# Kernel optimization log

Measured on AMD Instinct MI355X. Metric: run time of the kernel, lower is better.

## Reference

```python
import jax, jax.numpy as jnp
import numpy as np

B, S, D, H = 2, 2048, 1024, 16
HD = D // H
EPS = 1e-5

def gelu_tanh(x):
    # GPT-2 tanh approximation of GELU
    c = np.sqrt(2.0 / np.pi).astype(np.float32)
    return 0.5 * x * (1.0 + jnp.tanh(c * (x + 0.044715 * x * x * x)))

def layernorm(x, gamma, beta):
    mu = jnp.mean(x, axis=-1, keepdims=True)
    var = jnp.mean(jnp.square(x - mu), axis=-1, keepdims=True)
    return (x - mu) * jax.lax.rsqrt(var + EPS) * gamma + beta

def setup_inputs() -> dict:
    key = jax.random.key(0)
    ks = jax.random.split(key, 16)
    std = 0.02
    def w(k, shape):
        return jax.random.normal(k, shape, dtype=jnp.float32) * std
    return {
        "x": jax.random.normal(ks[0], (B, S, D), dtype=jnp.float32),
        "Wq": w(ks[1], (D, D)), "bq": jnp.zeros((D,), jnp.float32),
        "Wk": w(ks[2], (D, D)), "bk": jnp.zeros((D,), jnp.float32),
        "Wv": w(ks[3], (D, D)), "bv": jnp.zeros((D,), jnp.float32),
        "Wp": w(ks[4], (D, D)), "bp": jnp.zeros((D,), jnp.float32),
        "g0": jnp.ones((D,), jnp.float32), "beta0": jnp.zeros((D,), jnp.float32),
        "W1": w(ks[5], (D, 4 * D)), "b1": jnp.zeros((4 * D,), jnp.float32),
        "W2": w(ks[6], (4 * D, D)), "b2": jnp.zeros((D,), jnp.float32),
        "g1": jnp.ones((D,), jnp.float32), "beta1": jnp.zeros((D,), jnp.float32),
    }

def reference(x, Wq, bq, Wk, bk, Wv, bv, Wp, bp, g0, beta0, W1, b1, W2, b2, g1, beta1):
    b, s, d = x.shape
    # --- causal self-attention (naive full score matrix, as in source) ---
    q = (x @ Wq + bq).reshape(b, s, H, HD).transpose(0, 2, 1, 3)  # [b,h,s,hd]
    k = (x @ Wk + bk).reshape(b, s, H, HD).transpose(0, 2, 1, 3)
    v = (x @ Wv + bv).reshape(b, s, H, HD).transpose(0, 2, 1, 3)
    scores = jnp.einsum('bhqd,bhkd->bhqk', q, k) * (1.0 / np.sqrt(HD))
    mask = jnp.tril(jnp.ones((s, s), dtype=x.dtype))  # lower-triangular causal mask
    scores = scores * mask - 1e10 * (1.0 - mask)
    attn = jax.nn.softmax(scores, axis=-1)
    y = jnp.einsum('bhqk,bhkd->bhqd', attn, v)
    y = y.transpose(0, 2, 1, 3).reshape(b, s, d)
    a = y @ Wp + bp
    # --- post-LN MLP block ---
    x = x + a
    h = layernorm(x, g0, beta0)
    h = gelu_tanh(h @ W1 + b1)
    h = h @ W2 + b2
    x = x + h
    return layernorm(x, g1, beta1)
```

## Files before the change

### kernel.cpp

```cpp
#include <hip/hip_runtime.h>
#include <stdint.h>

#define S_LEN 2048
#define DIM   1024
#define NH    16
#define HDIM  64
#define MTOK  4096
#define DFF   4096

#define QS 0.18033688011112042f

typedef short bf16x8 __attribute__((ext_vector_type(8)));
typedef float f32x4  __attribute__((ext_vector_type(4)));
typedef float f32x16 __attribute__((ext_vector_type(16)));
typedef unsigned int u32x4 __attribute__((ext_vector_type(4)));

__device__ __forceinline__ unsigned short f2bf(float f) {
  unsigned int u = __float_as_uint(f);
  u += 0x7fffu + ((u >> 16) & 1u);
  return (unsigned short)(u >> 16);
}

__device__ __forceinline__ unsigned cvtpk(float a, float b) {
  unsigned r;
  asm("v_cvt_pk_bf16_f32 %0, %1, %2" : "=v"(r) : "v"(a), "v"(b));
  return r;
}

__device__ __forceinline__ float gelu_f(float x) {
  const float c = 0.7978845608028654f;
  float u = c * (x + 0.044715f * x * x * x);
  return 0.5f * x * (1.0f + tanhf(u));
}

__device__ __forceinline__ void gld_lds16(const void* g, void* lds) {
  using gu32p = __attribute__((address_space(1))) unsigned int*;
  using lu32p = __attribute__((address_space(3))) unsigned int*;
  __builtin_amdgcn_global_load_lds((gu32p)g, (lu32p)lds, 16, 0, 0);
}

__global__ __launch_bounds__(256) void cast_f32_bf16(const float* __restrict__ x,
                                                     unsigned short* __restrict__ xb) {
  const size_t i = (size_t)blockIdx.x * 256 + threadIdx.x;
  const float4 a = ((const float4*)x)[2 * i];
  const float4 b = ((const float4*)x)[2 * i + 1];
  ushort4 p0, p1;
  p0.x = f2bf(a.x); p0.y = f2bf(a.y); p0.z = f2bf(a.z); p0.w = f2bf(a.w);
  p1.x = f2bf(b.x); p1.y = f2bf(b.y); p1.z = f2bf(b.z); p1.w = f2bf(b.w);
  ((ushort4*)xb)[2 * i]     = p0;
  ((ushort4*)xb)[2 * i + 1] = p1;
}

__global__ __launch_bounds__(256) void tcast_k(const float* __restrict__ W,
                                               unsigned short* __restrict__ Wt,
                                               int K, int N, float scale) {
  __shared__ float tile[32][33];
  const int tx = threadIdx.x & 31, ty = threadIdx.x >> 5;
  const int n0 = blockIdx.x * 32, k0 = blockIdx.y * 32;
#pragma unroll
  for (int i = 0; i < 4; i++)
    tile[ty + 8 * i][tx] = W[(size_t)(k0 + ty + 8 * i) * N + n0 + tx];
  __syncthreads();
#pragma unroll
  for (int i = 0; i < 4; i++)
    Wt[(size_t)(n0 + ty + 8 * i) * K + k0 + tx] = f2bf(tile[tx][ty + 8 * i] * scale);
}

__global__ __launch_bounds__(256) void bcat_k(const float* __restrict__ bq,
                                              const float* __restrict__ bk,
                                              const float* __restrict__ bv,
                                              float* __restrict__ bqkv) {
  const int t = blockIdx.x * 256 + threadIdx.x;
  float v;
  if (t < 1024)      v = bq[t] * QS;
  else if (t < 2048) v = bk[t - 1024];
  else               v = bv[t - 2048];
  bqkv[t] = v;
}

__global__ __launch_bounds__(256) void vtrans_k(const unsigned short* __restrict__ qkv,
                                                unsigned short* __restrict__ vT) {
  __shared__ unsigned short tile[64][65];
  const int bh = blockIdx.y, b = bh >> 4, h = bh & 15;
  const int s0 = blockIdx.x * 64;
  const int t = threadIdx.x;
#pragma unroll
  for (int i = 0; i < 16; i++) {
    int idx = i * 256 + t, r = idx >> 6, c = idx & 63;
    tile[r][c] = qkv[(size_t)(b * S_LEN + s0 + r) * 3072 + 2048 + h * HDIM + c];
  }
  __syncthreads();
#pragma unroll
  for (int i = 0; i < 16; i++) {
    int idx = i * 256 + t, d = idx >> 6, s = idx & 63;
    vT[(size_t)(bh * HDIM + d) * S_LEN + s0 + s] = tile[s][d];
  }
}

template <int EPI>
__global__ __launch_bounds__(256, 2) void gemm2p(const unsigned short* __restrict__ A,
                                                 const unsigned short* __restrict__ Bt,
                                                 const float* __restrict__ bias,
                                                 const float* __restrict__ resid,
                                                 void* __restrict__ Cout,
                                                 int M, int N, int K) {
  __shared__ alignas(16) short As[2][128 * 64];
  __shared__ alignas(16) short Bs[2][128 * 64];
  const int t = threadIdx.x, w = t >> 6, lane = t & 63;

  const int gx = gridDim.x, nwg = gx * gridDim.y;
  const int bid = blockIdx.x + gx * blockIdx.y;
  const int swz = (bid & 7) * (nwg >> 3) + (bid >> 3);
  const int m0 = (swz / gx) * 128, n0 = (swz % gx) * 128;

  const int wr = (w >> 1) * 64, wc = (w & 1) * 64;
  const int lr = lane & 15, lg = lane >> 4;

  f32x4 acc[4][4] = {};

  const int sr = w * 32 + (lane >> 3);
  const int sc = (lane & 7) * 8;
  const unsigned short* Ag = A + (size_t)(m0 + sr) * K + sc;
  const unsigned short* Bg = Bt + (size_t)(n0 + sr) * K + sc;
  const int dbase = w * 4096 + lane * 16;

  const int NT = K >> 6;

#pragma unroll
  for (int i = 0; i < 4; i++) {
    gld_lds16(Ag + (size_t)(i * 8) * K, (char*)As[0] + dbase + i * 1024);
    gld_lds16(Bg + (size_t)(i * 8) * K, (char*)Bs[0] + dbase + i * 1024);
  }
  __syncthreads();

  int cur = 0;
  for (int kt = 0; kt < NT; ++kt) {
    if (kt + 1 < NT) {
      const int k1 = (kt + 1) << 6;
#pragma unroll
      for (int i = 0; i < 4; i++) {
        gld_lds16(Ag + (size_t)(i * 8) * K + k1, (char*)As[cur ^ 1] + dbase + i * 1024);
        gld_lds16(Bg + (size_t)(i * 8) * K + k1, (char*)Bs[cur ^ 1] + dbase + i * 1024);
      }
    }
    bf16x8 af[2][4], bfr[2][4];
#pragma unroll
    for (int ks = 0; ks < 2; ks++)
#pragma unroll
      for (int i = 0; i < 4; i++) {
        af[ks][i]  = *reinterpret_cast<const bf16x8*>(&As[cur][(wr + i * 16 + lr) * 64 + ks * 32 + lg * 8]);
        bfr[ks][i] = *reinterpret_cast<const bf16x8*>(&Bs[cur][(wc + i * 16 + lr) * 64 + ks * 32 + lg * 8]);
      }
    __builtin_amdgcn_s_setprio(1);
#pragma unroll
    for (int ks = 0; ks < 2; ks++)
#pragma unroll
      for (int mi = 0; mi < 4; mi++)
#pragma unroll
        for (int ni = 0; ni < 4; ni++)
          acc[mi][ni] = __builtin_amdgcn_mfma_f32_16x16x32_bf16(af[ks][mi], bfr[ks][ni],
                                                                acc[mi][ni], 0, 0, 0);
    __builtin_amdgcn_s_setprio(0);
    __syncthreads();
    cur ^= 1;
  }

  const int colb = n0 + wc + lr;
  const int rowb = m0 + wr + lg * 4;
#pragma unroll
  for (int ni = 0; ni < 4; ni++) {
    const int col = colb + ni * 16;
    const float bv = bias[col];
#pragma unroll
    for (int mi = 0; mi < 4; mi++) {
#pragma unroll
      for (int j = 0; j < 4; j++) {
        const int row = rowb + mi * 16 + j;
        const size_t idx = (size_t)row * N + col;
        float v = acc[mi][ni][j] + bv;
        if constexpr (EPI == 0) {
          ((unsigned short*)Cout)[idx] = f2bf(v);
        } else if constexpr (EPI == 1) {
          ((unsigned short*)Cout)[idx] = f2bf(gelu_f(v));
        } else {
          ((float*)Cout)[idx] = v + resid[idx];
        }
      }
    }
  }
}

__global__ __launch_bounds__(128) void attn32_k(const unsigned short* __restrict__ qkv,
                                                const unsigned short* __restrict__ vT,
                                                unsigned short* __restrict__ y) {
  __shared__ float smem[2][64][33];
  __shared__ float msh[2][64], lsh[2][64];

  const int t = threadIdx.x, w = t >> 6, lane = t & 63;
  const int ql = lane & 31, hi = lane >> 5;
  const int bh = blockIdx.x, bb = bh >> 4, hh = bh & 15;
  const int qt = 63 - blockIdx.y;
  const int half = w;
  const int q0 = qt * 32;

  const unsigned short* qp = qkv + (size_t)(bb * S_LEN + q0 + ql) * 3072 + hh * HDIM + hi * 8;
  const bf16x8 qf0 = *(const bf16x8*)(qp);
  const bf16x8 qf1 = *(const bf16x8*)(qp + 16);
  const bf16x8 qf2 = *(const bf16x8*)(qp + 32);
  const bf16x8 qf3 = *(const bf16x8*)(qp + 48);

  const unsigned short* kbp = qkv + (size_t)(bb * S_LEN) * 3072 + 1024 + hh * HDIM + hi * 8;
  const unsigned short* vbp = vT + (size_t)(bh * HDIM + ql) * (size_t)S_LEN + hi * 8;

  f32x16 acc0 = {}, acc1 = {};
  float m = -1e30f, l = 0.f;

  const int start = half * 32;

  const unsigned short* kp0 = kbp + (size_t)(start + ql) * 3072;
  bf16x8 kc0 = *(const bf16x8*)(kp0);
  bf16x8 kc1 = *(const bf16x8*)(kp0 + 16);
  bf16x8 kc2 = *(const bf16x8*)(kp0 + 32);
  bf16x8 kc3 = *(const bf16x8*)(kp0 + 48);

  for (int t0 = start; t0 <= q0; t0 += 64) {
    const unsigned short* vp = vbp + t0;
    const bf16x8 vf0 = *(const bf16x8*)(vp);
    const bf16x8 vf1 = *(const bf16x8*)(vp + 32 * S_LEN);
    const bf16x8 vf2 = *(const bf16x8*)(vp + 16);
    const bf16x8 vf3 = *(const bf16x8*)(vp + 32 * S_LEN + 16);

    __builtin_amdgcn_s_setprio(1);
    f32x16 st = {};
    st = __builtin_amdgcn_mfma_f32_32x32x16_bf16(kc0, qf0, st, 0, 0, 0);
    st = __builtin_amdgcn_mfma_f32_32x32x16_bf16(kc1, qf1, st, 0, 0, 0);
    st = __builtin_amdgcn_mfma_f32_32x32x16_bf16(kc2, qf2, st, 0, 0, 0);
    st = __builtin_amdgcn_mfma_f32_32x32x16_bf16(kc3, qf3, st, 0, 0, 0);
    __builtin_amdgcn_s_setprio(0);

    const int t1 = (t0 + 64 <= q0) ? (t0 + 64) : t0;
    const unsigned short* kpn = kbp + (size_t)(t1 + ql) * 3072;
    const bf16x8 kn0 = *(const bf16x8*)(kpn);
    const bf16x8 kn1 = *(const bf16x8*)(kpn + 16);
    const bf16x8 kn2 = *(const bf16x8*)(kpn + 32);
    const bf16x8 kn3 = *(const bf16x8*)(kpn + 48);

    if (t0 == q0) {
#pragma unroll
      for (int r = 0; r < 16; r++) {
        const int key = (r & 3) + 8 * (r >> 2) + 4 * hi;
        if (key > ql) st[r] = -1e30f;
      }
    }
    float pm = st[0];
#pragma unroll
    for (int r = 1; r < 16; r++) pm = fmaxf(pm, st[r]);
    pm = fmaxf(pm, __shfl_xor(pm, 32));
    if (!__all(pm - m <= 8.f)) {
      const float mn = fmaxf(m, pm);
      const float rs = exp2f(m - mn);
      l *= rs;
#pragma unroll
      for (int r = 0; r < 16; r++) { acc0[r] *= rs; acc1[r] *= rs; }
      m = mn;
    }
    float sum = 0.f;
#pragma unroll
    for (int r = 0; r < 16; r++) { st[r] = exp2f(st[r] - m); sum += st[r]; }
    sum += __shfl_xor(sum, 32);
    l += sum;

    {
      const unsigned c0 = cvtpk(st[0], st[1]), c1 = cvtpk(st[2], st[3]);
      const unsigned c2 = cvtpk(st[4], st[5]), c3 = cvtpk(st[6], st[7]);
      const unsigned x0 = __shfl_xor(c0, 32), x1 = __shfl_xor(c1, 32);
      const unsigned x2 = __shfl_xor(c2, 32), x3 = __shfl_xor(c3, 32);
      u32x4 fu;
      fu.x = hi ? x2 : c0; fu.y = hi ? x3 : c1;
      fu.z = hi ? c2 : x0; fu.w = hi ? c3 : x1;
      const bf16x8 pf = __builtin_bit_cast(bf16x8, fu);
      __builtin_amdgcn_s_setprio(1);
      acc0 = __builtin_amdgcn_mfma_f32_32x32x16_bf16(vf0, pf, acc0, 0, 0, 0);
      acc1 = __builtin_amdgcn_mfma_f32_32x32x16_bf16(vf1, pf, acc1, 0, 0, 0);
      __builtin_amdgcn_s_setprio(0);
    }
    {
      const unsigned c4 = cvtpk(st[8], st[9]),   c5 = cvtpk(st[10], st[11]);
      const unsigned c6 = cvtpk(st[12], st[13]), c7 = cvtpk(st[14], st[15]);
      const unsigned x4 = __shfl_xor(c4, 32), x5 = __shfl_xor(c5, 32);
      const unsigned x6 = __shfl_xor(c6, 32), x7 = __shfl_xor(c7, 32);
      u32x4 fu;
      fu.x = hi ? x6 : c4; fu.y = hi ? x7 : c5;
      fu.z = hi ? c6 : x4; fu.w = hi ? c7 : x5;
      const bf16x8 pf = __builtin_bit_cast(bf16x8, fu);
      __builtin_amdgcn_s_setprio(1);
      acc0 = __builtin_amdgcn_mfma_f32_32x32x16_bf16(vf2, pf, acc0, 0, 0, 0);
      acc1 = __builtin_amdgcn_mfma_f32_32x32x16_bf16(vf3, pf, acc1, 0, 0, 0);
      __builtin_amdgcn_s_setprio(0);
    }
    kc0 = kn0; kc1 = kn1; kc2 = kn2; kc3 = kn3;
  }

#pragma unroll
  for (int r = 0; r < 16; r++) {
    smem[w][lane][r]      = acc0[r];
    smem[w][lane][16 + r] = acc1[r];
  }
  msh[w][lane] = m; lsh[w][lane] = l;
  __syncthreads();
  if (half) return;

  const int pw = w ^ 1;
  const float mB = msh[pw][lane], lB = lsh[pw][lane];
  const float mm = fmaxf(m, mB);
  float sA = exp2f(m - mm), sB = exp2f(mB - mm);
  const float linv = 1.f / (l * sA + lB * sB);
  sA *= linv; sB *= linv;

  unsigned* tp = (unsigned*)&smem[w][0][0];
  const float* pa = &smem[pw][lane][0];
#pragma unroll
  for (int j = 0; j < 8; j++) {
    const int wd = (j & 1) + 4 * (j >> 1) + 2 * hi;
    const float a0 = acc0[2 * j] * sA + pa[2 * j] * sB;
    const float b0 = acc0[2 * j + 1] * sA + pa[2 * j + 1] * sB;
    tp[ql * 34 + wd] = cvtpk(a0, b0);
    const float a1 = acc1[2 * j] * sA + pa[16 + 2 * j] * sB;
    const float b1 = acc1[2 * j + 1] * sA + pa[16 + 2 * j + 1] * sB;
    tp[ql * 34 + 16 + wd] = cvtpk(a1, b1);
  }
  unsigned* yu = (unsigned*)y;
  const size_t yrow = (size_t)(bb * S_LEN + q0 + ql) * (DIM / 2) + hh * (HDIM / 2) + hi * 16;
#pragma unroll
  for (int i = 0; i < 8; i++) {
    const uint2 d2 = *(const uint2*)&tp[ql * 34 + hi * 16 + 2 * i];
    *(uint2*)&yu[yrow + 2 * i] = d2;
  }
}

template <int OUTBF>
__global__ __launch_bounds__(256) void ln_k(const float* __restrict__ X,
                                            const float* __restrict__ g,
                                            const float* __restrict__ be,
                                            void* __restrict__ out) {
  const int row = blockIdx.x, t = threadIdx.x;
  const float4 v = ((const float4*)(X + (size_t)row * DIM))[t];
  float s  = v.x + v.y + v.z + v.w;
  float s2 = v.x * v.x + v.y * v.y + v.z * v.z + v.w * v.w;
#pragma unroll
  for (int o = 32; o >= 1; o >>= 1) {
    s  += __shfl_down(s, o);
    s2 += __shfl_down(s2, o);
  }
  __shared__ float red[8];
  if ((t & 63) == 0) { red[t >> 6] = s; red[4 + (t >> 6)] = s2; }
  __syncthreads();
  s  = red[0] + red[1] + red[2] + red[3];
  s2 = red[4] + red[5] + red[6] + red[7];
  const float mu  = s * (1.0f / DIM);
  const float var = s2 * (1.0f / DIM) - mu * mu;
  const float r   = rsqrtf(var + 1e-5f);
  const float4 gv = ((const float4*)g)[t];
  const float4 bv = ((const float4*)be)[t];
  const float o0 = (v.x - mu) * r * gv.x + bv.x;
  const float o1 = (v.y - mu) * r * gv.y + bv.y;
  const float o2 = (v.z - mu) * r * gv.z + bv.z;
  const float o3 = (v.w - mu) * r * gv.w + bv.w;
  if constexpr (OUTBF) {
    ushort4 p; p.x = f2bf(o0); p.y = f2bf(o1); p.z = f2bf(o2); p.w = f2bf(o3);
    ((ushort4*)out)[(size_t)row * 256 + t] = p;
  } else {
    float4 p; p.x = o0; p.y = o1; p.z = o2; p.w = o3;
    ((float4*)out)[(size_t)row * 256 + t] = p;
  }
}

extern "C" void kernel_launch(void* const* d_in, const int* in_sizes, int n_in,
                              void* d_out, int out_size, void* d_ws, size_t ws_size,
                              hipStream_t stream) {
  const float* x   = (const float*)d_in[0];
  const float* Wq  = (const float*)d_in[1];
  const float* bq  = (const float*)d_in[2];
  const float* Wk  = (const float*)d_in[3];
  const float* bk  = (const float*)d_in[4];
  const float* Wv  = (const float*)d_in[5];
  const float* bv  = (const float*)d_in[6];
  const float* Wp  = (const float*)d_in[7];
  const float* bp  = (const float*)d_in[8];
  const float* g0  = (const float*)d_in[9];
  const float* be0 = (const float*)d_in[10];
  const float* W1  = (const float*)d_in[11];
  const float* b1  = (const float*)d_in[12];
  const float* W2  = (const float*)d_in[13];
  const float* b2  = (const float*)d_in[14];
  const float* g1  = (const float*)d_in[15];
  const float* be1 = (const float*)d_in[16];

  char* ws = (char*)d_ws;
  const size_t MB = 1ull << 20;
  unsigned short* xb    = (unsigned short*)(ws + 0 * MB);
  unsigned short* qkvb  = (unsigned short*)(ws + 8 * MB);
  unsigned short* vTb   = (unsigned short*)(ws + 32 * MB);
  unsigned short* yb    = (unsigned short*)(ws + 40 * MB);
  float*          bqkv  = (float*)(ws + 48 * MB);
  float*          x1    = (float*)(ws + 48 * MB);
  unsigned short* hb    = (unsigned short*)(ws + 64 * MB);
  unsigned short* WqkvT = (unsigned short*)(ws + 72 * MB);
  unsigned short* WpT   = (unsigned short*)(ws + 78 * MB);
  unsigned short* W1T   = (unsigned short*)(ws + 80 * MB);
  unsigned short* W2T   = (unsigned short*)(ws + 88 * MB);
  unsigned short* h1    = (unsigned short*)(ws + 8 * MB);
  float*          x2    = (float*)(ws + 64 * MB);

  cast_f32_bf16<<<2048, 256, 0, stream>>>(x, xb);
  tcast_k<<<dim3(32, 32), 256, 0, stream>>>(Wq, WqkvT,               1024, 1024, QS);
  tcast_k<<<dim3(32, 32), 256, 0, stream>>>(Wk, WqkvT + 1024 * 1024, 1024, 1024, 1.f);
  tcast_k<<<dim3(32, 32), 256, 0, stream>>>(Wv, WqkvT + 2048 * 1024, 1024, 1024, 1.f);
  tcast_k<<<dim3(32, 32), 256, 0, stream>>>(Wp, WpT, 1024, 1024, 1.f);
  tcast_k<<<dim3(128, 32), 256, 0, stream>>>(W1, W1T, 1024, 4096, 1.f);
  tcast_k<<<dim3(32, 128), 256, 0, stream>>>(W2, W2T, 4096, 1024, 1.f);
  bcat_k<<<12, 256, 0, stream>>>(bq, bk, bv, bqkv);

  gemm2p<0><<<dim3(24, 32), 256, 0, stream>>>(xb, WqkvT, bqkv, nullptr, qkvb, MTOK, 3072, 1024);

  vtrans_k<<<dim3(32, 32), 256, 0, stream>>>(qkvb, vTb);
  attn32_k<<<dim3(32, 64), 128, 0, stream>>>(qkvb, vTb, yb);

  gemm2p<2><<<dim3(8, 32), 256, 0, stream>>>(yb, WpT, bp, x, x1, MTOK, DIM, DIM);
  ln_k<1><<<4096, 256, 0, stream>>>(x1, g0, be0, hb);

  gemm2p<1><<<dim3(32, 32), 256, 0, stream>>>(hb, W1T, b1, nullptr, h1, MTOK, DFF, DIM);
  gemm2p<2><<<dim3(8, 32), 256, 0, stream>>>(h1, W2T, b2, x1, x2, MTOK, DIM, DFF);
  ln_k<0><<<4096, 256, 0, stream>>>(x2, g1, be1, d_out);
}
```

Before: 462.1 us.

## Split-K the N=1024 GEMMs with atomic accumulation and finer vmcnt waits

The two output-projection GEMMs with N=1024 (Wp and W2) now split K across two grid slices. Each slice atomically adds its partial sums into an fp32 output that a new kernel pre-fills with residual plus bias. This doubles the workgroup count from 256 to 512 so more CUs have work. The main loop also replaces __syncthreads with an explicit vmcnt wait plus raw s_barrier, so the next tile's prefetch can stay in flight while the current one is consumed. The cost is two extra elementwise passes, atomic traffic, and nondeterministic summation order.

Result: no change. 461.0 us (-0.2%).

```diff
diff --git a/kernel.cpp b/kernel.cpp
--- a/kernel.cpp
+++ b/kernel.cpp
@@ -78,6 +78,17 @@
   bqkv[t] = v;
 }
 
+__global__ __launch_bounds__(256) void resinit_k(const float* __restrict__ X,
+                                                 const float* __restrict__ b,
+                                                 float* __restrict__ out) {
+  const int row = blockIdx.x, t = threadIdx.x;
+  const float4 xv = ((const float4*)(X + (size_t)row * DIM))[t];
+  const float4 bv = ((const float4*)b)[t];
+  float4 o;
+  o.x = xv.x + bv.x; o.y = xv.y + bv.y; o.z = xv.z + bv.z; o.w = xv.w + bv.w;
+  ((float4*)(out + (size_t)row * DIM))[t] = o;
+}
+
 __global__ __launch_bounds__(256) void vtrans_k(const unsigned short* __restrict__ qkv,
                                                 unsigned short* __restrict__ vT) {
   __shared__ unsigned short tile[64][65];
@@ -101,7 +112,6 @@
 __global__ __launch_bounds__(256, 2) void gemm2p(const unsigned short* __restrict__ A,
                                                  const unsigned short* __restrict__ Bt,
                                                  const float* __restrict__ bias,
-                                                 const float* __restrict__ resid,
                                                  void* __restrict__ Cout,
                                                  int M, int N, int K) {
   __shared__ alignas(16) short As[2][128 * 64];
@@ -124,25 +134,31 @@
   const unsigned short* Bg = Bt + (size_t)(n0 + sr) * K + sc;
   const int dbase = w * 4096 + lane * 16;
 
-  const int NT = K >> 6;
+  const int Ks = K / gridDim.z;
+  const int kbase = blockIdx.z * Ks;
+  const int NT = Ks >> 6;
 
 #pragma unroll
   for (int i = 0; i < 4; i++) {
-    gld_lds16(Ag + (size_t)(i * 8) * K, (char*)As[0] + dbase + i * 1024);
-    gld_lds16(Bg + (size_t)(i * 8) * K, (char*)Bs[0] + dbase + i * 1024);
-  }
-  __syncthreads();
+    gld_lds16(Ag + (size_t)(i * 8) * K + kbase, (char*)As[0] + dbase + i * 1024);
+    gld_lds16(Bg + (size_t)(i * 8) * K + kbase, (char*)Bs[0] + dbase + i * 1024);
+  }
 
   int cur = 0;
   for (int kt = 0; kt < NT; ++kt) {
     if (kt + 1 < NT) {
-      const int k1 = (kt + 1) << 6;
+      const int k1 = kbase + ((kt + 1) << 6);
 #pragma unroll
       for (int i = 0; i < 4; i++) {
         gld_lds16(Ag + (size_t)(i * 8) * K + k1, (char*)As[cur ^ 1] + dbase + i * 1024);
         gld_lds16(Bg + (size_t)(i * 8) * K + k1, (char*)Bs[cur ^ 1] + dbase + i * 1024);
       }
-    }
+      asm volatile("s_waitcnt vmcnt(8)" ::: "memory");
+    } else {
+      asm volatile("s_waitcnt vmcnt(0)" ::: "memory");
+    }
+    __builtin_amdgcn_s_barrier();
+
     bf16x8 af[2][4], bfr[2][4];
 #pragma unroll
     for (int ks = 0; ks < 2; ks++)
@@ -161,7 +177,7 @@
           acc[mi][ni] = __builtin_amdgcn_mfma_f32_16x16x32_bf16(af[ks][mi], bfr[ks][ni],
                                                                 acc[mi][ni], 0, 0, 0);
     __builtin_amdgcn_s_setprio(0);
-    __syncthreads();
+    __builtin_amdgcn_s_barrier();
     cur ^= 1;
   }
 
@@ -170,7 +186,7 @@
 #pragma unroll
   for (int ni = 0; ni < 4; ni++) {
     const int col = colb + ni * 16;
-    const float bv = bias[col];
+    const float bv = (EPI == 3) ? 0.f : bias[col];
 #pragma unroll
     for (int mi = 0; mi < 4; mi++) {
 #pragma unroll
@@ -183,7 +199,7 @@
         } else if constexpr (EPI == 1) {
           ((unsigned short*)Cout)[idx] = f2bf(gelu_f(v));
         } else {
-          ((float*)Cout)[idx] = v + resid[idx];
+          unsafeAtomicAdd((float*)Cout + idx, v);
         }
       }
     }
@@ -421,15 +437,17 @@
   tcast_k<<<dim3(32, 128), 256, 0, stream>>>(W2, W2T, 4096, 1024, 1.f);
   bcat_k<<<12, 256, 0, stream>>>(bq, bk, bv, bqkv);
 
-  gemm2p<0><<<dim3(24, 32), 256, 0, stream>>>(xb, WqkvT, bqkv, nullptr, qkvb, MTOK, 3072, 1024);
+  gemm2p<0><<<dim3(24, 32, 1), 256, 0, stream>>>(xb, WqkvT, bqkv, qkvb, MTOK, 3072, 1024);
 
   vtrans_k<<<dim3(32, 32), 256, 0, stream>>>(qkvb, vTb);
   attn32_k<<<dim3(32, 64), 128, 0, stream>>>(qkvb, vTb, yb);
 
-  gemm2p<2><<<dim3(8, 32), 256, 0, stream>>>(yb, WpT, bp, x, x1, MTOK, DIM, DIM);
+  resinit_k<<<4096, 256, 0, stream>>>(x, bp, x1);
+  gemm2p<3><<<dim3(8, 32, 2), 256, 0, stream>>>(yb, WpT, nullptr, x1, MTOK, DIM, DIM);
   ln_k<1><<<4096, 256, 0, stream>>>(x1, g0, be0, hb);
 
-  gemm2p<1><<<dim3(32, 32), 256, 0, stream>>>(hb, W1T, b1, nullptr, h1, MTOK, DFF, DIM);
-  gemm2p<2><<<dim3(8, 32), 256, 0, stream>>>(h1, W2T, b2, x1, x2, MTOK, DIM, DFF);
+  gemm2p<1><<<dim3(32, 32, 1), 256, 0, stream>>>(hb, W1T, b1, h1, MTOK, DFF, DIM);
+  resinit_k<<<4096, 256, 0, stream>>>(x1, b2, x2);
+  gemm2p<3><<<dim3(8, 32, 2), 256, 0, stream>>>(h1, W2T, nullptr, x2, MTOK, DIM, DFF);
   ln_k<0><<<4096, 256, 0, stream>>>(x2, g1, be1, d_out);
 }
```
